# Kernel tuning notes

Measured on AMD Instinct MI355X. Metric: run time of the kernel, lower is better.

Reference implementation:

```python
import jax, jax.numpy as jnp
import numpy as np

B, N, K = 4, 8192, 16
FEAT = 512
GRID = 45
M = GRID * GRID


def _p(key, shape, scale=0.05):
    return jax.random.normal(key, shape, dtype=jnp.float32) * scale


def setup_inputs() -> dict:
    key = jax.random.key(0)
    ks = jax.random.split(key, 40)
    inp = {"pts": jax.random.normal(ks[0], (B, N, 3), dtype=jnp.float32)}
    specs = {
        "w1": (64, 12), "b1": (64,), "w2": (64, 64), "b2": (64,), "w3": (64, 64), "b3": (64,),
        "g1a": (64, 64), "g1ab": (64,), "g1b": (128, 64), "g1bb": (128,),
        "g2a": (128, 128), "g2ab": (128,), "g2b": (1024, 128), "g2bb": (1024,),
        "m1": (FEAT, 1024), "m1b": (FEAT,), "m2": (FEAT, FEAT), "m2b": (FEAT,),
        "f1a": (FEAT, FEAT + 2), "f1ab": (FEAT,), "f1b": (FEAT, FEAT), "f1bb": (FEAT,), "f1c": (3, FEAT), "f1cb": (3,),
        "f2a": (FEAT, FEAT + 3), "f2ab": (FEAT,), "f2b": (FEAT, FEAT), "f2bb": (FEAT,), "f2c": (3, FEAT), "f2cb": (3,),
    }
    for i, (name, shp) in enumerate(specs.items()):
        inp[name] = _p(ks[i + 1], shp)
    return inp


def conv1x1(x, w, b):
    # x: (B,C,N), w: (Cout,Cin), b: (Cout,)
    return jnp.einsum('bcn,oc->bon', x, w) + b[None, :, None]


def knn_idx(x, k):
    # x: (B,C,N) -> neighbor indices (B,N,k) by smallest squared distance (self included)
    xt = jnp.swapaxes(x, 1, 2)                      # (B,N,C)
    sq = jnp.sum(xt * xt, axis=-1)                  # (B,N)
    inner = jnp.einsum('bnc,bmc->bnm', xt, xt)      # (B,N,N)
    neg_d2 = 2.0 * inner - sq[:, :, None] - sq[:, None, :]
    return jax.lax.top_k(neg_d2, k)[1]


def gather_nbrs(feats_t, idx):
    # feats_t: (B,N,C), idx: (B,N,k) -> (B,N,k,C)
    return jax.vmap(lambda f, i: f[i])(feats_t, idx)


def local_maxpool(x, idx):
    # x: (B,C,N) -> (B,C,N) max over k neighbors
    nb = gather_nbrs(jnp.swapaxes(x, 1, 2), idx)    # (B,N,k,C)
    return jnp.swapaxes(jnp.max(nb, axis=2), 1, 2)


def local_cov(pts_t, idx):
    # pts_t: (B,3,N) -> (B,12,N): coords + outer product of first two neighbors
    p = jnp.swapaxes(pts_t, 1, 2)                   # (B,N,3)
    nb = gather_nbrs(p, idx)                        # (B,N,k,3)
    outer = nb[:, :, 0, :, None] * nb[:, :, 1, None, :]   # (B,N,3,3)
    feat = jnp.concatenate([p, outer.reshape(p.shape[0], p.shape[1], 9)], axis=-1)
    return jnp.swapaxes(feat, 1, 2)


def _forward(pts, w1, b1, w2, b2, w3, b3, g1a, g1ab, g1b, g1bb, g2a, g2ab, g2b, g2bb,
             m1, m1b, m2, m2b, f1a, f1ab, f1b, f1bb, f1c, f1cb, f2a, f2ab, f2b, f2bb, f2c, f2cb):
    relu = jax.nn.relu
    pts_t = jnp.swapaxes(pts, 1, 2)                 # (B,3,N)
    # ---- encoder ----
    idx = knn_idx(pts_t, K)
    x = local_cov(pts_t, idx)                       # (B,12,N)
    x = relu(conv1x1(x, w1, b1))
    x = relu(conv1x1(x, w2, b2))
    x = relu(conv1x1(x, w3, b3))                    # (B,64,N)
    idx = knn_idx(x, K)
    g = local_maxpool(x, idx)
    g = conv1x1(relu(conv1x1(g, g1a, g1ab)), g1b, g1bb)   # (B,128,N)
    idx = knn_idx(g, K)
    h = local_maxpool(g, idx)
    h = conv1x1(relu(conv1x1(h, g2a, g2ab)), g2b, g2bb)   # (B,1024,N)
    glob = jnp.max(h, axis=2, keepdims=True)        # (B,1024,1)
    code = conv1x1(relu(conv1x1(glob, m1, m1b)), m2, m2b)  # (B,FEAT,1)
    # ---- decoder ----
    Bs = code.shape[0]
    cw = jnp.broadcast_to(code, (Bs, FEAT, M))
    lin = jnp.linspace(-0.3, 0.3, GRID, dtype=jnp.float32)
    gx, gy = jnp.meshgrid(lin, lin, indexing='ij')
    grid = jnp.stack([gx.ravel(), gy.ravel()], axis=0)     # (2,M)
    grid = jnp.broadcast_to(grid[None], (Bs, 2, M))

    def fold(points, wa, ba, wb, bb, wc, bc):
        y = jnp.concatenate([cw, points], axis=1)
        y = relu(conv1x1(y, wa, ba))
        y = relu(conv1x1(y, wb, bb))
        return conv1x1(y, wc, bc)                    # (B,3,M)

    mid = fold(grid, f1a, f1ab, f1b, f1bb, f1c, f1cb)
    rec = fold(mid, f2a, f2ab, f2b, f2bb, f2c, f2cb)
    return jnp.swapaxes(rec, 1, 2)                   # (B,M,3)


def reference(pts, w1, b1, w2, b2, w3, b3, g1a, g1ab, g1b, g1bb, g2a, g2ab, g2b, g2bb,
              m1, m1b, m2, m2b, f1a, f1ab, f1b, f1bb, f1c, f1cb, f2a, f2ab, f2b, f2bb, f2c, f2cb):
    return _forward(pts, w1, b1, w2, b2, w3, b3, g1a, g1ab, g1b, g1bb, g2a, g2ab, g2b, g2bb,
                    m1, m1b, m2, m2b, f1a, f1ab, f1b, f1bb, f1c, f1cb, f2a, f2ab, f2b, f2bb, f2c, f2cb)
```

## Files before the change

kernel.cpp:

```cpp
#include <hip/hip_runtime.h>
#include <stdint.h>

#define B_ 4
#define N_ 8192
#define K_ 16
#define FEAT_ 512
#define GRID_ 45
#define M_ (GRID_*GRID_)

typedef unsigned long long ull;
typedef __bf16 bf16x8 __attribute__((ext_vector_type(8)));
typedef float f32x16 __attribute__((ext_vector_type(16)));


__device__ __forceinline__ unsigned int fmap(float f){
  unsigned int u = __float_as_uint(f);
  return (u & 0x80000000u) ? ~u : (u | 0x80000000u);
}
__device__ __forceinline__ float funmap(unsigned int u){
  return (u & 0x80000000u) ? __uint_as_float(u ^ 0x80000000u) : __uint_as_float(~u);
}

__device__ __forceinline__ void ins16(ull (&d)[16], ull k){
  if (k < d[15]){
    bool c[16];
#pragma unroll
    for (int s = 0; s < 16; ++s) c[s] = k < d[s];
#pragma unroll
    for (int s = 15; s >= 1; --s) d[s] = c[s-1] ? d[s-1] : (c[s] ? k : d[s]);
    if (c[0]) d[0] = k;
  }
}

__device__ __forceinline__ void ins16b(unsigned (&dk)[16], unsigned (&di)[16],
                                       unsigned k, unsigned id){
  if (k < dk[15]){
    bool c[16];
#pragma unroll
    for (int s = 0; s < 16; ++s) c[s] = k < dk[s];
#pragma unroll
    for (int s = 15; s >= 1; --s){
      dk[s] = c[s-1] ? dk[s-1] : (c[s] ? k  : dk[s]);
      di[s] = c[s-1] ? di[s-1] : (c[s] ? id : di[s]);
    }
    if (c[0]){ dk[0] = k; di[0] = id; }
  }
}

__device__ __forceinline__ void bsplit(float x, unsigned short& h, unsigned short& l){
  __bf16 hh = (__bf16)x;
  __bf16 ll = (__bf16)(x - (float)hh);
  h = __builtin_bit_cast(unsigned short, hh);
  l = __builtin_bit_cast(unsigned short, ll);
}

#define GLDS16(l, g) __builtin_amdgcn_global_load_lds((const __attribute__((address_space(1))) void*)(g), (__attribute__((address_space(3))) void*)(l), 16, 0, 0)
#define GLDS4(l, g)  __builtin_amdgcn_global_load_lds((const __attribute__((address_space(1))) void*)(g), (__attribute__((address_space(3))) void*)(l), 4, 0, 0)

#define KEY_INF 0xFF800000FFFFFFFFull

__global__ void k_init(unsigned int* glob){
  int i = blockIdx.x*256 + threadIdx.x;
  if (i < B_*1024) glob[i] = 0x007FFFFFu;
}

__global__ __launch_bounds__(256) void k_nn1(const float* __restrict__ pts,
                                             unsigned long long* __restrict__ nn64){
  __shared__ __align__(16) float sp4[2048][4];
  int b = blockIdx.z, s = blockIdx.y;
  int c0 = s*2048;
  const float* P = pts + (size_t)b*N_*3;
  for (int p = threadIdx.x; p < 2048; p += 256){
    const float* src = P + (size_t)(c0 + p)*3;
    sp4[p][0] = src[0]; sp4[p][1] = src[1]; sp4[p][2] = src[2]; sp4[p][3] = 0.f;
  }
  __syncthreads();
  int n = blockIdx.x*256 + threadIdx.x;
  float qx = P[n*3], qy = P[n*3+1], qz = P[n*3+2];
  float best = 1e30f; int bi = 0;
  for (int j = 0; j < 2048; ++j){
    float4 sv = *(const float4*)sp4[j];
    float dx = qx - sv.x, dy = qy - sv.y, dz = qz - sv.z;
    float d2 = fmaf(dx,dx, fmaf(dy,dy, dz*dz));
    int cj = c0 + j;
    if (d2 < best && cj != n){ best = d2; bi = cj; }
  }
  unsigned long long key = ((unsigned long long)__float_as_uint(best) << 32) | (unsigned int)bi;
  atomicMin(&nn64[(size_t)b*N_ + n], key);
}

__global__ __launch_bounds__(256) void k_cov_mlp(const float* __restrict__ pts,
    const unsigned long long* __restrict__ nn64,
    const float* __restrict__ w1, const float* __restrict__ b1,
    const float* __restrict__ w2, const float* __restrict__ b2,
    const float* __restrict__ w3, const float* __restrict__ b3,
    float* __restrict__ xout, unsigned short* __restrict__ T,
    float* __restrict__ cc){
  __shared__ __align__(16) float W1t[12*64];
  __shared__ __align__(16) float W2t[64*64];
  __shared__ __align__(16) float W3t[64*64];
  __shared__ float B1[64], B2[64], B3[64];
  __shared__ __align__(16) float x0[64][12];
  __shared__ __align__(16) float h1[64][64];
  __shared__ __align__(16) float h2[64][64];
  int b = blockIdx.y; int n0 = blockIdx.x*64; int tid = threadIdx.x;
  for (int i = tid; i < 12*64; i += 256){ int o = i % 64, ci = i / 64; W1t[i] = w1[o*12 + ci]; }
  for (int i = tid; i < 64*64; i += 256){ int o = i % 64, ci = i / 64; W2t[i] = w2[o*64 + ci]; W3t[i] = w3[o*64 + ci]; }
  if (tid < 64){ B1[tid]=b1[tid]; B2[tid]=b2[tid]; B3[tid]=b3[tid]; }
  {
    int p = tid % 64, cg = tid / 64;
    int n = n0 + p;
    const float* P = pts + ((size_t)b*N_ + n)*3;
    int nb = (int)(nn64[(size_t)b*N_ + n] & 0xFFFFFFFFull);
    const float* Q = pts + ((size_t)b*N_ + nb)*3;
    if (cg == 0){ x0[p][0]=P[0]; x0[p][1]=P[1]; x0[p][2]=P[2]; }
    else { int i = cg-1; float pi = P[i];
      x0[p][3+i*3+0]=pi*Q[0]; x0[p][3+i*3+1]=pi*Q[1]; x0[p][3+i*3+2]=pi*Q[2]; }
  }
  __syncthreads();
  { int o = tid % 64, pg = tid / 64;
    for (int p = pg; p < 64; p += 4){
      float acc = B1[o];
#pragma unroll
      for (int ci = 0; ci < 12; ++ci) acc = fmaf(W1t[ci*64+o], x0[p][ci], acc);
      h1[p][o] = fmaxf(acc, 0.f);
    } }
  __syncthreads();
  { int o = tid % 64, pg = tid / 64;
    for (int p = pg; p < 64; p += 4){
      float acc = B2[o];
#pragma unroll
      for (int ci = 0; ci < 64; ++ci) acc = fmaf(W2t[ci*64+o], h1[p][ci], acc);
      h2[p][o] = fmaxf(acc, 0.f);
    } }
  __syncthreads();
  { int o = tid % 64, pg = tid / 64;
    for (int p = pg; p < 64; p += 4){
      float acc = B3[o];
#pragma unroll
      for (int ci = 0; ci < 64; ++ci) acc = fmaf(W3t[ci*64+o], h2[p][ci], acc);
      float r = fmaxf(acc, 0.f);
      xout[((size_t)b*N_ + n0 + p)*64 + o] = r;
      h1[p][o] = r;
    } }
  __syncthreads();
  {
    char* Tb = (char*)T;
    const size_t HS = (size_t)N_*16, PS = 2*HS, KS = 4*HS;
    const size_t Bb = (size_t)b*4*KS;
    for (int e = tid; e < 64*8; e += 256){
      int p = e >> 3, gg = e & 7;
      int kf = gg >> 1, h = gg & 1;
      unsigned short hs[8], ls[8];
#pragma unroll
      for (int j = 0; j < 8; ++j) bsplit(h1[p][gg*8+j], hs[j], ls[j]);
      size_t base = Bb + (size_t)kf*KS + (size_t)h*HS + (size_t)(n0+p)*16;
      *(uint4*)(Tb + base)      = *(uint4*)hs;
      *(uint4*)(Tb + base + PS) = *(uint4*)ls;
    }
    if (tid < 64){
      float ss = 0.f;
#pragma unroll 8
      for (int c = 0; c < 64; ++c){ float v = h1[tid][(c + tid) & 63]; ss = fmaf(v, v, ss); }
      cc[(size_t)b*N_ + n0 + tid] = ss;
    }
  }
}

template<int KF>
__global__ __launch_bounds__(256) void k_prep4(const float* __restrict__ f,
    unsigned short* __restrict__ T, float* __restrict__ cc){
  int b = blockIdx.y; int n = blockIdx.x*256 + threadIdx.x;
  const float* src = f + ((size_t)b*N_ + n)*(KF*16);
  char* Tb = (char*)T;
  float ss = 0.f;
#pragma unroll
  for (int kf = 0; kf < KF; ++kf){
    float v[16];
#pragma unroll
    for (int c4 = 0; c4 < 4; ++c4){
      float4 t4 = *(const float4*)&src[kf*16 + c4*4];
      v[c4*4]=t4.x; v[c4*4+1]=t4.y; v[c4*4+2]=t4.z; v[c4*4+3]=t4.w;
    }
    unsigned short hs[16], ls[16];
#pragma unroll
    for (int c = 0; c < 16; ++c){
      float x = v[c];
      ss = fmaf(x, x, ss);
      bsplit(x, hs[c], ls[c]);
    }
    size_t base = ((((size_t)b*KF + kf)*2)*2)*(size_t)(N_*16) + (size_t)n*16;
    const size_t HS = (size_t)N_*16;
    const size_t PS = 2*HS;
    *(uint4*)(Tb + base)            = *(uint4*)&hs[0];
    *(uint4*)(Tb + base + HS)       = *(uint4*)&hs[8];
    *(uint4*)(Tb + base + PS)       = *(uint4*)&ls[0];
    *(uint4*)(Tb + base + PS + HS)  = *(uint4*)&ls[8];
  }
  cc[(size_t)b*N_ + n] = ss;
}

template<int KF, int MW, int S>
__global__ __launch_bounds__(256, MW) void k_knnF(const unsigned short* __restrict__ T,
    const float* __restrict__ ccg, ull* __restrict__ qkeys){
  extern __shared__ char smem[];
  constexpr int NT = (N_/S)/64;
  char* As = smem;
  char* Cs = smem + KF*4096;

  const int tid = threadIdx.x, lane = tid & 63, wid = tid >> 6;
  const int hi = lane >> 5, l31 = lane & 31;
  const int b = blockIdx.z, sp = blockIdx.y, q0 = blockIdx.x*128;
  const int c0 = sp*(N_/S);
  const char* Tb = (const char*)T;
  const size_t HS = (size_t)N_*16, PS = 2*HS, KS = 4*HS;
  const size_t Bb = (size_t)b*KF*KS;
  const float* ccb = ccg + (size_t)b*N_;

  const int q = q0 + wid*32 + l31;
  bf16x8 qh[KF], ql[KF];
#pragma unroll
  for (int kf = 0; kf < KF; ++kf){
    size_t o = Bb + kf*KS + hi*HS + (size_t)q*16;
    qh[kf] = *(const bf16x8*)(Tb + o);
    ql[kf] = *(const bf16x8*)(Tb + o + PS);
  }

  unsigned dk[16], di[16];
#pragma unroll
  for (int t = 0; t < 16; ++t){ dk[t] = 0xFFFFFFFFu; di[t] = 0xFFFFFFFFu; }
  float kapf = __builtin_inff();

  auto stage = [&](int t0){
#pragma unroll
    for (int si = 0; si < KF; ++si){
      int s = wid + 4*si;
      int kf = s >> 2, pl = (s >> 1) & 1, h = s & 1;
      GLDS16(As + s*1024,
             Tb + Bb + kf*KS + pl*PS + h*HS + (size_t)(c0 + t0)*16);
    }
    if (wid == 0) GLDS4(Cs, (const char*)(ccb + c0 + t0));
  };

  for (int t = 0; t < NT; ++t){
    const int t0 = t*64;
    __syncthreads();
    stage(t0);
    asm volatile("s_waitcnt vmcnt(0)" ::: "memory");
    __syncthreads();

    const char* Ab = As + hi*1024 + l31*16;
    const float* cct = (const float*)Cs;
#pragma unroll
    for (int i = 0; i < 2; ++i){
      f32x16 acc = (f32x16)(0.f);
#pragma unroll
      for (int kf = 0; kf < KF; ++kf){
        bf16x8 ah = *(const bf16x8*)(Ab + kf*4096 + i*512);
        bf16x8 al = *(const bf16x8*)(Ab + kf*4096 + 2048 + i*512);
        acc = __builtin_amdgcn_mfma_f32_32x32x16_bf16(ah, qh[kf], acc, 0, 0, 0);
        acc = __builtin_amdgcn_mfma_f32_32x32x16_bf16(ah, ql[kf], acc, 0, 0, 0);
        acc = __builtin_amdgcn_mfma_f32_32x32x16_bf16(al, qh[kf], acc, 0, 0, 0);
      }
#pragma unroll
      for (int rq = 0; rq < 4; ++rq){
        float4 c4 = *(const float4*)(cct + i*32 + 4*hi + 8*rq);
        int rowb = c0 + t0 + i*32 + 4*hi + 8*rq;
        float v0 = fmaf(-2.f, acc[rq*4+0], c4.x);
        float v1 = fmaf(-2.f, acc[rq*4+1], c4.y);
        float v2 = fmaf(-2.f, acc[rq*4+2], c4.z);
        float v3 = fmaf(-2.f, acc[rq*4+3], c4.w);
        if (fminf(fminf(v0, v1), fminf(v2, v3)) < kapf){
          if (v0 < kapf) ins16b(dk, di, fmap(v0), (unsigned)(rowb+0));
          if (v1 < kapf) ins16b(dk, di, fmap(v1), (unsigned)(rowb+1));
          if (v2 < kapf) ins16b(dk, di, fmap(v2), (unsigned)(rowb+2));
          if (v3 < kapf) ins16b(dk, di, fmap(v3), (unsigned)(rowb+3));
          unsigned kk = dk[15];
          kapf = (kk >= 0xFF800000u) ? __builtin_inff() : funmap(kk);
        }
      }
    }
  }
  ull* op = qkeys + (((size_t)((size_t)b*N_ + q)*S + sp)*2 + hi)*16;
#pragma unroll
  for (int t = 0; t < 16; ++t) op[t] = ((ull)dk[t] << 32) | di[t];
}

template<int S>
__global__ void k_sel(const ull* __restrict__ qkeys, int* __restrict__ idxout){
  int i = blockIdx.x*256 + threadIdx.x;
  if (i >= B_*N_) return;
  ull best[16];
#pragma unroll
  for (int t = 0; t < 16; ++t) best[t] = KEY_INF;
  const ull* kp = qkeys + (size_t)i*(S*32);
  for (int t = 0; t < S*32; ++t) ins16(best, kp[t]);
  int* op = idxout + (size_t)i*16;
#pragma unroll
  for (int t = 0; t < 16; ++t) op[t] = (int)(best[t] & 0xffffffffu);
}

__global__ __launch_bounds__(256) void k_gpool_mlp(const float* __restrict__ x,
    const int* __restrict__ idx,
    const float* __restrict__ g1a, const float* __restrict__ g1ab,
    const float* __restrict__ g1b, const float* __restrict__ g1bb,
    float* __restrict__ gout){
  __shared__ __align__(16) float Wt1[64*64];
  __shared__ __align__(16) float Wt2[64*128];
  __shared__ float Ba[64], Bb[128];
  __shared__ __align__(16) float m[64][64];
  __shared__ __align__(16) float r[64][64];
  int b = blockIdx.y; int n0 = blockIdx.x*64; int tid = threadIdx.x;
  for (int i = tid; i < 64*64; i += 256){ int o = i%64, ci = i/64; Wt1[i] = g1a[o*64+ci]; }
  for (int i = tid; i < 64*128; i += 256){ int o = i%128, ci = i/128; Wt2[i] = g1b[o*64+ci]; }
  if (tid < 64) Ba[tid] = g1ab[tid];
  if (tid < 128) Bb[tid] = g1bb[tid];
  { int p = tid/4, cg = tid%4; int n = n0 + p;
    const int* ip = idx + ((size_t)b*N_ + n)*16;
    float mm[16];
#pragma unroll
    for (int u = 0; u < 16; ++u) mm[u] = -1e30f;
    for (int k = 0; k < 16; ++k){
      int nb = ip[k];
      const float4* src = (const float4*)(x + ((size_t)b*N_ + nb)*64 + cg*16);
#pragma unroll
      for (int u = 0; u < 4; ++u){
        float4 v = src[u];
        mm[4*u  ] = fmaxf(mm[4*u  ], v.x); mm[4*u+1] = fmaxf(mm[4*u+1], v.y);
        mm[4*u+2] = fmaxf(mm[4*u+2], v.z); mm[4*u+3] = fmaxf(mm[4*u+3], v.w);
      }
    }
#pragma unroll
    for (int u = 0; u < 16; ++u) m[p][cg*16+u] = mm[u];
  }
  __syncthreads();
  { int o = tid%64, pg = tid/64;
    float acc[16];
#pragma unroll
    for (int u = 0; u < 16; ++u) acc[u] = Ba[o];
    for (int ci = 0; ci < 64; ci += 4){
      float w0 = Wt1[ci*64+o], w1_ = Wt1[(ci+1)*64+o], w2_ = Wt1[(ci+2)*64+o], w3_ = Wt1[(ci+3)*64+o];
#pragma unroll
      for (int u = 0; u < 16; ++u){
        float4 mv = *(const float4*)&m[pg*16+u][ci];
        acc[u] = fmaf(w0, mv.x, acc[u]); acc[u] = fmaf(w1_, mv.y, acc[u]);
        acc[u] = fmaf(w2_, mv.z, acc[u]); acc[u] = fmaf(w3_, mv.w, acc[u]);
      }
    }
#pragma unroll
    for (int u = 0; u < 16; ++u) r[pg*16+u][o] = fmaxf(acc[u], 0.f);
  }
  __syncthreads();
  { int o = tid%128, pg = tid/128;
    float acc[32];
#pragma unroll
    for (int u = 0; u < 32; ++u) acc[u] = Bb[o];
    for (int ci = 0; ci < 64; ci += 4){
      float w0 = Wt2[ci*128+o], w1_ = Wt2[(ci+1)*128+o], w2_ = Wt2[(ci+2)*128+o], w3_ = Wt2[(ci+3)*128+o];
#pragma unroll
      for (int u = 0; u < 32; ++u){
        float4 rv = *(const float4*)&r[pg*32+u][ci];
        acc[u] = fmaf(w0, rv.x, acc[u]); acc[u] = fmaf(w1_, rv.y, acc[u]);
        acc[u] = fmaf(w2_, rv.z, acc[u]); acc[u] = fmaf(w3_, rv.w, acc[u]);
      }
    }
#pragma unroll
    for (int u = 0; u < 32; ++u)
      gout[((size_t)b*N_ + n0 + pg*32 + u)*128 + o] = acc[u];
  }
}

__global__ __launch_bounds__(256) void k_hpool_max(const float* __restrict__ g,
    const int* __restrict__ idx,
    const float* __restrict__ g2a, const float* __restrict__ g2ab,
    const float* __restrict__ g2b, const float* __restrict__ g2bb,
    unsigned int* __restrict__ glob){
  __shared__ __align__(16) float m[32][128];
  __shared__ __align__(16) float t[32][128];
  int b = blockIdx.y; int n0 = blockIdx.x*32; int tid = threadIdx.x;
  { int p = tid/8, cg = tid%8; int n = n0+p;
    const int* ip = idx + ((size_t)b*N_+n)*16;
    float mm[16];
#pragma unroll
    for (int u = 0; u < 16; ++u) mm[u] = -1e30f;
    for (int k = 0; k < 16; ++k){
      int nb = ip[k];
      const float4* src = (const float4*)(g + ((size_t)b*N_+nb)*128 + cg*16);
#pragma unroll
      for (int u = 0; u < 4; ++u){
        float4 v = src[u];
        mm[4*u  ] = fmaxf(mm[4*u  ], v.x); mm[4*u+1] = fmaxf(mm[4*u+1], v.y);
        mm[4*u+2] = fmaxf(mm[4*u+2], v.z); mm[4*u+3] = fmaxf(mm[4*u+3], v.w);
      }
    }
#pragma unroll
    for (int u = 0; u < 16; ++u) m[p][cg*16+u] = mm[u];
  }
  __syncthreads();
  { int o = tid%128, pg = tid/128;
    float acc[16];
#pragma unroll
    for (int u = 0; u < 16; ++u) acc[u] = g2ab[o];
    const float4* wrow = (const float4*)(g2a + (size_t)o*128);
    for (int c4 = 0; c4 < 32; ++c4){
      float4 wv = wrow[c4];
#pragma unroll
      for (int u = 0; u < 16; ++u){
        float4 mv = *(const float4*)&m[pg*16+u][c4*4];
        acc[u] = fmaf(wv.x,mv.x,acc[u]); acc[u] = fmaf(wv.y,mv.y,acc[u]);
        acc[u] = fmaf(wv.z,mv.z,acc[u]); acc[u] = fmaf(wv.w,mv.w,acc[u]);
      }
    }
#pragma unroll
    for (int u = 0; u < 16; ++u) t[pg*16+u][o] = fmaxf(acc[u], 0.f);
  }
  __syncthreads();
  for (int oc = 0; oc < 4; ++oc){
    int o = oc*256 + tid;
    const float4* wrow = (const float4*)(g2b + (size_t)o*128);
    float acc[32];
#pragma unroll
    for (int u = 0; u < 32; ++u) acc[u] = 0.f;
    for (int c4 = 0; c4 < 32; ++c4){
      float4 wv = wrow[c4];
#pragma unroll
      for (int u = 0; u < 32; ++u){
        float4 tv = *(const float4*)&t[u][c4*4];
        acc[u] = fmaf(wv.x,tv.x,acc[u]); acc[u] = fmaf(wv.y,tv.y,acc[u]);
        acc[u] = fmaf(wv.z,tv.z,acc[u]); acc[u] = fmaf(wv.w,tv.w,acc[u]);
      }
    }
    float bias = g2bb[o];
    float mx = -1e30f;
#pragma unroll
    for (int u = 0; u < 32; ++u) mx = fmaxf(mx, acc[u] + bias);
    atomicMax(&glob[b*1024 + o], fmap(mx));
  }
}

__global__ __launch_bounds__(512) void k_code(const unsigned int* __restrict__ glob,
    const float* __restrict__ m1, const float* __restrict__ m1b,
    const float* __restrict__ m2, const float* __restrict__ m2b,
    const float* __restrict__ f1a, const float* __restrict__ f1ab,
    const float* __restrict__ f2a, const float* __restrict__ f2ab,
    float* __restrict__ base1, float* __restrict__ base2){
  __shared__ __align__(16) float gl_s[1024];
  __shared__ __align__(16) float hid_s[512];
  __shared__ __align__(16) float code_s[512];
  int b = blockIdx.x; int tid = threadIdx.x;
  for (int i = tid; i < 1024; i += 512) gl_s[i] = funmap(glob[b*1024+i]);
  __syncthreads();
  { float acc = m1b[tid];
    const float4* wr = (const float4*)(m1 + (size_t)tid*1024);
    for (int c4 = 0; c4 < 256; ++c4){ float4 wv = wr[c4]; float4 gv = *(const float4*)&gl_s[c4*4];
      acc = fmaf(wv.x,gv.x,acc); acc = fmaf(wv.y,gv.y,acc);
      acc = fmaf(wv.z,gv.z,acc); acc = fmaf(wv.w,gv.w,acc); }
    hid_s[tid] = fmaxf(acc, 0.f);
  }
  __syncthreads();
  { float acc = m2b[tid];
    const float4* wr = (const float4*)(m2 + (size_t)tid*512);
    for (int c4 = 0; c4 < 128; ++c4){ float4 wv = wr[c4]; float4 hv = *(const float4*)&hid_s[c4*4];
      acc = fmaf(wv.x,hv.x,acc); acc = fmaf(wv.y,hv.y,acc);
      acc = fmaf(wv.z,hv.z,acc); acc = fmaf(wv.w,hv.w,acc); }
    code_s[tid] = acc;
  }
  __syncthreads();
  { float acc = f1ab[tid];
    const float* wr = f1a + (size_t)tid*514;
    for (int c = 0; c < 512; ++c) acc = fmaf(wr[c], code_s[c], acc);
    base1[b*512 + tid] = acc;
  }
  { float acc = f2ab[tid];
    const float* wr = f2a + (size_t)tid*515;
    for (int c = 0; c < 512; ++c) acc = fmaf(wr[c], code_s[c], acc);
    base2[b*512 + tid] = acc;
  }
}

template<int NIN>
__global__ __launch_bounds__(256) void k_fold(const float* __restrict__ base,
    const float* __restrict__ fa,
    const float* __restrict__ fb, const float* __restrict__ fbb,
    const float* __restrict__ fc, const float* __restrict__ fcb,
    const float* __restrict__ pin, float* __restrict__ pout){
  __shared__ __align__(16) float y1[16][512];
  __shared__ __align__(16) float y2[16][516];
  __shared__ float pcoord[16][NIN];
  int b = blockIdx.y; int m0 = blockIdx.x*16; int tid = threadIdx.x;
  if (tid < 16*NIN){
    int p = tid / NIN, c = tid % NIN;
    int mm = min(m0 + p, M_-1);
    float v;
    if (NIN == 2){
      const float step = 0.6f/44.f;
      int ii = (c == 0) ? (mm/GRID_) : (mm%GRID_);
      v = -0.3f + step*ii;
    } else {
      v = pin[((size_t)b*M_ + mm)*3 + c];
    }
    pcoord[p][c] = v;
  }
  __syncthreads();
  const int stride_a = 512 + NIN;
  for (int rep = 0; rep < 2; ++rep){
    int o = rep*256 + tid;
    float av[NIN];
#pragma unroll
    for (int c = 0; c < NIN; ++c) av[c] = fa[(size_t)o*stride_a + 512 + c];
    float bv = base[b*512 + o];
#pragma unroll
    for (int p = 0; p < 16; ++p){
      float acc = bv;
#pragma unroll
      for (int c = 0; c < NIN; ++c) acc = fmaf(av[c], pcoord[p][c], acc);
      y1[p][o] = fmaxf(acc, 0.f);
    }
  }
  __syncthreads();
  for (int rep = 0; rep < 2; ++rep){
    int o2 = rep*256 + tid;
    const float* wr = fb + (size_t)o2*512;
    float acc[16];
#pragma unroll
    for (int u = 0; u < 16; ++u) acc[u] = 0.f;
    for (int c4 = 0; c4 < 128; ++c4){
      float4 wv = *(const float4*)&wr[c4*4];
#pragma unroll
      for (int u = 0; u < 16; ++u){
        float4 yv = *(const float4*)&y1[u][c4*4];
        acc[u] = fmaf(wv.x,yv.x,acc[u]); acc[u] = fmaf(wv.y,yv.y,acc[u]);
        acc[u] = fmaf(wv.z,yv.z,acc[u]); acc[u] = fmaf(wv.w,yv.w,acc[u]);
      }
    }
    float bias = fbb[o2];
#pragma unroll
    for (int u = 0; u < 16; ++u) y2[u][o2] = fmaxf(acc[u] + bias, 0.f);
  }
  __syncthreads();
  if (tid < 48){
    int p = tid / 3, c = tid % 3;
    const float* wr = fc + (size_t)c*512;
    float acc = fcb[c];
    for (int o4 = 0; o4 < 128; ++o4){
      float4 wv = *(const float4*)&wr[o4*4];
      float4 yv = *(const float4*)&y2[p][o4*4];
      acc = fmaf(wv.x,yv.x,acc); acc = fmaf(wv.y,yv.y,acc);
      acc = fmaf(wv.z,yv.z,acc); acc = fmaf(wv.w,yv.w,acc);
    }
    int mm = m0 + p;
    if (mm < M_) pout[((size_t)b*M_ + mm)*3 + c] = acc;
  }
}

extern "C" void kernel_launch(void* const* d_in, const int* in_sizes, int n_in,
                              void* d_out, int out_size, void* d_ws, size_t ws_size,
                              hipStream_t stream){
  const float* pts  = (const float*)d_in[0];
  const float* w1   = (const float*)d_in[1];  const float* b1   = (const float*)d_in[2];
  const float* w2   = (const float*)d_in[3];  const float* b2   = (const float*)d_in[4];
  const float* w3   = (const float*)d_in[5];  const float* b3   = (const float*)d_in[6];
  const float* g1a  = (const float*)d_in[7];  const float* g1ab = (const float*)d_in[8];
  const float* g1b  = (const float*)d_in[9];  const float* g1bb = (const float*)d_in[10];
  const float* g2a  = (const float*)d_in[11]; const float* g2ab = (const float*)d_in[12];
  const float* g2b  = (const float*)d_in[13]; const float* g2bb = (const float*)d_in[14];
  const float* m1   = (const float*)d_in[15]; const float* m1b  = (const float*)d_in[16];
  const float* m2   = (const float*)d_in[17]; const float* m2b  = (const float*)d_in[18];
  const float* f1a  = (const float*)d_in[19]; const float* f1ab = (const float*)d_in[20];
  const float* f1b  = (const float*)d_in[21]; const float* f1bb = (const float*)d_in[22];
  const float* f1c  = (const float*)d_in[23]; const float* f1cb = (const float*)d_in[24];
  const float* f2a  = (const float*)d_in[25]; const float* f2ab = (const float*)d_in[26];
  const float* f2b  = (const float*)d_in[27]; const float* f2bb = (const float*)d_in[28];
  const float* f2c  = (const float*)d_in[29]; const float* f2cb = (const float*)d_in[30];
  float* out = (float*)d_out;

  char* w = (char*)d_ws;
  auto alloc = [&](size_t bytes){ char* p = w; w += (bytes + 255) & ~(size_t)255; return p; };
  unsigned long long* nn64 = (unsigned long long*)alloc((size_t)B_*N_*8);
  float* x    = (float*)alloc((size_t)B_*N_*64*4);
  float* g    = (float*)alloc((size_t)B_*N_*128*4);
  unsigned short* T64  = (unsigned short*)alloc((size_t)B_*4*4*N_*16);
  unsigned short* T128 = (unsigned short*)alloc((size_t)B_*8*4*N_*16);
  float* ccf  = (float*)alloc((size_t)B_*N_*4);
  int*   idx  = (int*)alloc((size_t)B_*N_*16*4);
  ull*   qkeys = (ull*)alloc((size_t)B_*N_*4*2*16*8);
  unsigned int* glob = (unsigned int*)alloc((size_t)B_*1024*4);
  float* base1 = (float*)alloc((size_t)B_*512*4);
  float* base2 = (float*)alloc((size_t)B_*512*4);
  float* mid   = (float*)alloc((size_t)B_*M_*3*4);
  (void)ws_size; (void)in_sizes; (void)n_in; (void)out_size;

  const int SMEM4 = 4*4096 + 256;
  const int SMEM8 = 8*4096 + 256;
  hipFuncSetAttribute((const void*)k_knnF<4,4,4>, hipFuncAttributeMaxDynamicSharedMemorySize, SMEM4);
  hipFuncSetAttribute((const void*)k_knnF<8,3,4>, hipFuncAttributeMaxDynamicSharedMemorySize, SMEM8);

  hipMemsetAsync(nn64, 0xFF, (size_t)B_*N_*8, stream);
  k_init<<<dim3((B_*1024+255)/256), 256, 0, stream>>>(glob);
  k_nn1<<<dim3(N_/256, 4, B_), 256, 0, stream>>>(pts, nn64);
  k_cov_mlp<<<dim3(N_/64, B_), 256, 0, stream>>>(pts, nn64, w1,b1,w2,b2,w3,b3, x, T64, ccf);

  k_knnF<4,4,4><<<dim3(N_/128, 4, B_), 256, SMEM4, stream>>>(T64, ccf, qkeys);
  k_sel<4><<<dim3(B_*N_/256), 256, 0, stream>>>(qkeys, idx);

  k_gpool_mlp<<<dim3(N_/64, B_), 256, 0, stream>>>(x, idx, g1a,g1ab,g1b,g1bb, g);

  k_prep4<8><<<dim3(N_/256, B_), 256, 0, stream>>>(g, T128, ccf);
  k_knnF<8,3,4><<<dim3(N_/128, 4, B_), 256, SMEM8, stream>>>(T128, ccf, qkeys);
  k_sel<4><<<dim3(B_*N_/256), 256, 0, stream>>>(qkeys, idx);

  k_hpool_max<<<dim3(N_/32, B_), 256, 0, stream>>>(g, idx, g2a,g2ab,g2b,g2bb, glob);
  k_code<<<dim3(B_), 512, 0, stream>>>(glob, m1,m1b,m2,m2b, f1a,f1ab, f2a,f2ab, base1, base2);
  k_fold<2><<<dim3((M_+15)/16, B_), 256, 0, stream>>>(base1, f1a, f1b, f1bb, f1c, f1cb, nullptr, mid);
  k_fold<3><<<dim3((M_+15)/16, B_), 256, 0, stream>>>(base2, f2a, f2b, f2bb, f2c, f2cb, mid, out);
}
```

Measured before the change: 1.638 ms.

## Halve KNN column splits and merge candidate lists with bitonic merge

```diff
diff --git a/kernel.cpp b/kernel.cpp
--- a/kernel.cpp
+++ b/kernel.cpp
@@ -21,17 +21,6 @@
   return (u & 0x80000000u) ? __uint_as_float(u ^ 0x80000000u) : __uint_as_float(~u);
 }
 
-__device__ __forceinline__ void ins16(ull (&d)[16], ull k){
-  if (k < d[15]){
-    bool c[16];
-#pragma unroll
-    for (int s = 0; s < 16; ++s) c[s] = k < d[s];
-#pragma unroll
-    for (int s = 15; s >= 1; --s) d[s] = c[s-1] ? d[s-1] : (c[s] ? k : d[s]);
-    if (c[0]) d[0] = k;
-  }
-}
-
 __device__ __forceinline__ void ins16b(unsigned (&dk)[16], unsigned (&di)[16],
                                        unsigned k, unsigned id){
   if (k < dk[15]){
@@ -45,6 +34,29 @@
     }
     if (c[0]){ dk[0] = k; di[0] = id; }
   }
+}
+
+__device__ __forceinline__ void bsort16(ull (&c)[16]){
+#pragma unroll
+  for (int d = 8; d >= 1; d >>= 1){
+#pragma unroll
+    for (int i = 0; i < 16; ++i){
+      if (!(i & d)){
+        ull x = c[i], y = c[i|d];
+        bool lt = x < y;
+        c[i]   = lt ? x : y;
+        c[i|d] = lt ? y : x;
+      }
+    }
+  }
+}
+__device__ __forceinline__ void bmerge16(ull (&a)[16], const ull (&b)[16]){
+#pragma unroll
+  for (int i = 0; i < 16; ++i){
+    ull bv = b[15-i];
+    a[i] = a[i] < bv ? a[i] : bv;
+  }
+  bsort16(a);
 }
 
 __device__ __forceinline__ void bsplit(float x, unsigned short& h, unsigned short& l){
@@ -290,14 +302,19 @@
 __global__ void k_sel(const ull* __restrict__ qkeys, int* __restrict__ idxout){
   int i = blockIdx.x*256 + threadIdx.x;
   if (i >= B_*N_) return;
-  ull best[16];
-#pragma unroll
-  for (int t = 0; t < 16; ++t) best[t] = KEY_INF;
   const ull* kp = qkeys + (size_t)i*(S*32);
-  for (int t = 0; t < S*32; ++t) ins16(best, kp[t]);
+  ull a[16], t[16];
+#pragma unroll
+  for (int u = 0; u < 16; ++u) a[u] = kp[u];
+#pragma unroll
+  for (int r = 1; r < S*2; ++r){
+#pragma unroll
+    for (int u = 0; u < 16; ++u) t[u] = kp[r*16 + u];
+    bmerge16(a, t);
+  }
   int* op = idxout + (size_t)i*16;
 #pragma unroll
-  for (int t = 0; t < 16; ++t) op[t] = (int)(best[t] & 0xffffffffu);
+  for (int u = 0; u < 16; ++u) op[u] = (int)(a[u] & 0xffffffffu);
 }
 
 __global__ __launch_bounds__(256) void k_gpool_mlp(const float* __restrict__ x,
@@ -592,22 +609,22 @@
 
   const int SMEM4 = 4*4096 + 256;
   const int SMEM8 = 8*4096 + 256;
-  hipFuncSetAttribute((const void*)k_knnF<4,4,4>, hipFuncAttributeMaxDynamicSharedMemorySize, SMEM4);
-  hipFuncSetAttribute((const void*)k_knnF<8,3,4>, hipFuncAttributeMaxDynamicSharedMemorySize, SMEM8);
+  hipFuncSetAttribute((const void*)k_knnF<4,2,2>, hipFuncAttributeMaxDynamicSharedMemorySize, SMEM4);
+  hipFuncSetAttribute((const void*)k_knnF<8,2,2>, hipFuncAttributeMaxDynamicSharedMemorySize, SMEM8);
 
   hipMemsetAsync(nn64, 0xFF, (size_t)B_*N_*8, stream);
   k_init<<<dim3((B_*1024+255)/256), 256, 0, stream>>>(glob);
   k_nn1<<<dim3(N_/256, 4, B_), 256, 0, stream>>>(pts, nn64);
   k_cov_mlp<<<dim3(N_/64, B_), 256, 0, stream>>>(pts, nn64, w1,b1,w2,b2,w3,b3, x, T64, ccf);
 
-  k_knnF<4,4,4><<<dim3(N_/128, 4, B_), 256, SMEM4, stream>>>(T64, ccf, qkeys);
-  k_sel<4><<<dim3(B_*N_/256), 256, 0, stream>>>(qkeys, idx);
+  k_knnF<4,2,2><<<dim3(N_/128, 2, B_), 256, SMEM4, stream>>>(T64, ccf, qkeys);
+  k_sel<2><<<dim3(B_*N_/256), 256, 0, stream>>>(qkeys, idx);
 
   k_gpool_mlp<<<dim3(N_/64, B_), 256, 0, stream>>>(x, idx, g1a,g1ab,g1b,g1bb, g);
 
   k_prep4<8><<<dim3(N_/256, B_), 256, 0, stream>>>(g, T128, ccf);
-  k_knnF<8,3,4><<<dim3(N_/128, 4, B_), 256, SMEM8, stream>>>(T128, ccf, qkeys);
-  k_sel<4><<<dim3(B_*N_/256), 256, 0, stream>>>(qkeys, idx);
+  k_knnF<8,2,2><<<dim3(N_/128, 2, B_), 256, SMEM8, stream>>>(T128, ccf, qkeys);
+  k_sel<2><<<dim3(B_*N_/256), 256, 0, stream>>>(qkeys, idx);
 
   k_hpool_max<<<dim3(N_/32, B_), 256, 0, stream>>>(g, idx, g2a,g2ab,g2b,g2bb, glob);
   k_code<<<dim3(B_), 512, 0, stream>>>(glob, m1,m1b,m2,m2b, f1a,f1ab, f2a,f2ab, base1, base2);
```

Result: no change. 1.624 ms (-0.9%).
